# Kernel tuning notes

Hardware: AMD Instinct MI355X
Metric: run time of the kernel (lower is better)

Reference implementation:

```python
import jax, jax.numpy as jnp
import numpy as np

C = 64          # n_channels
NCLS = 10       # output_size
EPS = 1e-5      # GroupNorm eps (torch default)
T0, DT, NSTEPS = 0.0, 0.1, 10  # t0=0, t1=1, dt=0.1 -> 10 fixed RK4 steps


def _gn(x, w, b):
    # GroupNorm(C, C): per-sample, per-channel norm over H,W
    m = x.mean(axis=(2, 3), keepdims=True)
    v = ((x - m) ** 2).mean(axis=(2, 3), keepdims=True)
    return (x - m) * jax.lax.rsqrt(v + EPS) * w[None, :, None, None] + b[None, :, None, None]


def _conv(x, w, b, stride, pad):
    y = jax.lax.conv_general_dilated(x, w, (stride, stride), pad,
                                     dimension_numbers=('NCHW', 'OIHW', 'NCHW'))
    return y + b[None, :, None, None]


def setup_inputs() -> dict:
    key = jax.random.key(0)
    ks = jax.random.split(key, 8)
    rnd = lambda k, shape, s: jax.random.normal(k, shape, jnp.float32) * s
    B = 64
    return dict(
        x=jax.random.normal(ks[0], (B, 1, 130, 130), jnp.float32),
        # downsampler: Conv(1->C,3,1,VALID), GN, ReLU, Conv(C->C,4,2,1), GN, ReLU, Conv(C->C,4,2,1)
        ds_w1=rnd(ks[1], (C, 1, 3, 3), 0.2), ds_b1=jnp.zeros((C,), jnp.float32),
        ds_n1w=jnp.ones((C,), jnp.float32), ds_n1b=jnp.zeros((C,), jnp.float32),
        ds_w2=rnd(ks[2], (C, C, 4, 4), 0.03), ds_b2=jnp.zeros((C,), jnp.float32),
        ds_n2w=jnp.ones((C,), jnp.float32), ds_n2b=jnp.zeros((C,), jnp.float32),
        ds_w3=rnd(ks[3], (C, C, 4, 4), 0.03), ds_b3=jnp.zeros((C,), jnp.float32),
        # ODE RHS: two Conv2d(C+1 -> C, 3, 1, 1) with time channel concat, two GroupNorms
        ode_w1=rnd(ks[4], (C, C + 1, 3, 3), 0.04), ode_b1=jnp.zeros((C,), jnp.float32),
        ode_n1w=jnp.ones((C,), jnp.float32), ode_n1b=jnp.zeros((C,), jnp.float32),
        ode_w2=rnd(ks[5], (C, C + 1, 3, 3), 0.04), ode_b2=jnp.zeros((C,), jnp.float32),
        ode_n2w=jnp.ones((C,), jnp.float32), ode_n2b=jnp.zeros((C,), jnp.float32),
        # classification head: GN, ReLU, GAP, Linear(C -> 10)
        head_nw=jnp.ones((C,), jnp.float32), head_nb=jnp.zeros((C,), jnp.float32),
        head_W=rnd(ks[6], (NCLS, C), 0.1), head_b=jnp.zeros((NCLS,), jnp.float32),
    )


def reference(x, ds_w1, ds_b1, ds_n1w, ds_n1b, ds_w2, ds_b2, ds_n2w, ds_n2b, ds_w3, ds_b3,
              ode_w1, ode_b1, ode_n1w, ode_n1b, ode_w2, ode_b2, ode_n2w, ode_n2b,
              head_nw, head_nb, head_W, head_b):
    P1 = [(1, 1), (1, 1)]
    # ---- downsampler ----
    h = _conv(x, ds_w1, ds_b1, 1, 'VALID')                      # [B,C,128,128]
    h = jax.nn.relu(_gn(h, ds_n1w, ds_n1b))
    h = _conv(h, ds_w2, ds_b2, 2, P1)                           # [B,C,64,64]
    h = jax.nn.relu(_gn(h, ds_n2w, ds_n2b))
    h = _conv(h, ds_w3, ds_b3, 2, P1)                           # [B,C,32,32]

    # ---- ODE layer: fixed-step classic RK4 (tableau_low), 10 steps ----
    def rhs(t, z):
        z = jax.nn.relu(_gn(z, ode_n1w, ode_n1b))
        ts = jnp.full_like(z[:, :1], t)
        z = _conv(jnp.concatenate((ts, z), axis=1), ode_w1, ode_b1, 1, P1)
        z = jax.nn.relu(_gn(z, ode_n2w, ode_n2b))
        ts = jnp.full_like(z[:, :1], t)
        z = _conv(jnp.concatenate((ts, z), axis=1), ode_w2, ode_b2, 1, P1)
        return z

    def step(z, i):
        t = T0 + i * DT
        k1 = rhs(t, z)
        k2 = rhs(t + 0.5 * DT, z + 0.5 * DT * k1)
        k3 = rhs(t + 0.5 * DT, z + 0.5 * DT * k2)
        k4 = rhs(t + DT, z + DT * k3)
        return z + (DT / 6.0) * (k1 + 2.0 * k2 + 2.0 * k3 + k4), None

    h, _ = jax.lax.scan(step, h, jnp.arange(NSTEPS, dtype=jnp.float32))

    # ---- classification head ----
    h = jax.nn.relu(_gn(h, head_nw, head_nb))
    h = h.mean(axis=(2, 3))                                     # AdaptiveAvgPool2d((1,1)) + Flatten
    return h @ head_W.T + head_b                                # [B, 10]
```

## Files before the change

kernel.cpp:

```cpp
#include <hip/hip_runtime.h>

#define BB 64
#define CC 64

typedef __attribute__((ext_vector_type(8))) short short8;
typedef __attribute__((ext_vector_type(4))) short short4v;
typedef __attribute__((ext_vector_type(4))) float f32x4;

__device__ __forceinline__ float bf2f(unsigned short h) {
    unsigned int u = ((unsigned int)h) << 16;
    float f; __builtin_memcpy(&f, &u, 4); return f;
}
__device__ __forceinline__ unsigned short f2bf(float f) {
    unsigned int u; __builtin_memcpy(&u, &f, 4);
    u += 0x7fffu + ((u >> 16) & 1u);
    return (unsigned short)(u >> 16);
}

__global__ __launch_bounds__(256) void conv1stats_kernel(const float* __restrict__ x,
    const float* __restrict__ w1, const float* __restrict__ b1,
    float* __restrict__ ps, float* __restrict__ ps2) {
    __shared__ float sw1[576];
    __shared__ float sb1[64];
    __shared__ float xs[10 * 130];
    int tid = threadIdx.x;
    int qq = blockIdx.x;
    int b = blockIdx.y;
    for (int i = tid; i < 576; i += 256) sw1[i] = w1[i];
    if (tid < 64) sb1[tid] = b1[tid];
    const float* xb = x + (size_t)b * 130 * 130;
    int c = tid >> 2, q = tid & 3;
    float s = 0.f, s2 = 0.f;
    for (int sidx = 0; sidx < 2; sidx++) {
        int row0 = (qq * 2 + sidx) * 8;
        __syncthreads();
        for (int i = tid; i < 1300; i += 256) xs[i] = xb[row0 * 130 + i];
        __syncthreads();
        const float* wc = &sw1[c * 9];
        float bc = sb1[c];
        for (int p = q; p < 1024; p += 4) {
            int y = p >> 7, xx = p & 127;
            float v = bc;
#pragma unroll
            for (int ky = 0; ky < 3; ky++)
#pragma unroll
                for (int kx = 0; kx < 3; kx++)
                    v += xs[(y + ky) * 130 + xx + kx] * wc[ky * 3 + kx];
            s += v; s2 += v * v;
        }
    }
    s  += __shfl_xor(s, 1, 64);  s  += __shfl_xor(s, 2, 64);
    s2 += __shfl_xor(s2, 1, 64); s2 += __shfl_xor(s2, 2, 64);
    if (q == 0) {
        ps [(b * 8 + qq) * 64 + c] = s;
        ps2[(b * 8 + qq) * 64 + c] = s2;
    }
}

__global__ __launch_bounds__(256) void gn1fin_kernel(const float* __restrict__ ps,
    const float* __restrict__ ps2, const float* __restrict__ n1w, const float* __restrict__ n1b,
    float* __restrict__ gn1sc, float* __restrict__ gn1sh) {
    int i = blockIdx.x * 256 + threadIdx.x;
    if (i >= BB * CC) return;
    int c = i & 63, b = i >> 6;
    float s = 0.f, s2 = 0.f;
#pragma unroll
    for (int qq = 0; qq < 8; qq++) {
        s  += ps [(b * 8 + qq) * 64 + c];
        s2 += ps2[(b * 8 + qq) * 64 + c];
    }
    float mean = s / 16384.f;
    float var = s2 / 16384.f - mean * mean;
    float rstd = rsqrtf(var + 1e-5f);
    float sc = rstd * n1w[c];
    gn1sc[i] = sc;
    gn1sh[i] = n1b[c] - mean * sc;
}

__global__ __launch_bounds__(256) void prepack_kernel(const float* __restrict__ w1,
    const float* __restrict__ w2, const float* __restrict__ dw2,
    const float* __restrict__ dw3, unsigned short* __restrict__ Apk,
    float* __restrict__ Stab) {
    int set = blockIdx.y, kc = blockIdx.x, tid = threadIdx.x;
    int nchunk = (set < 2) ? 18 : 32;
    if (kc < nchunk) {
        const float* w = (set == 0) ? w1 : (set == 1) ? w2 : (set == 2) ? dw2 : dw3;
        size_t off = (set == 0) ? 0 : (set == 1) ? 36864 : (set == 2) ? 73728 : 139264;
        for (int e = tid; e < 2048; e += 256) {
            int co = e >> 5, j = e & 31;
            int k = kc * 32 + j;
            int ci = k & 63;
            int tap = k >> 6;
            float val;
            if (set < 2) val = w[(co * 65 + ci + 1) * 9 + tap];
            else         val = w[((co << 6) + ci) * 16 + tap];
            Apk[off + (size_t)kc * 2048 + e] = f2bf(val);
        }
    }
    if (set < 2 && kc == 0) {
        const float* w = set ? w2 : w1;
        for (int t = tid; t < 576; t += 256) {
            int co = t / 9, tap = t % 9;
            Stab[set * 576 + t] = w[(co * 65) * 9 + tap];
        }
    }
}

__global__ __launch_bounds__(256) void ds2mfma_kernel(const float* __restrict__ x,
    const float* __restrict__ w1, const float* __restrict__ b1,
    const float* __restrict__ gn1sc, const float* __restrict__ gn1sh,
    const unsigned short* __restrict__ Apk, const float* __restrict__ bias2,
    unsigned short* __restrict__ h2, float* __restrict__ sums_out) {
    __shared__ unsigned short X[2 * 198 * 64];
    __shared__ float xs[8 * 68];
    __shared__ float sw1[576];
    __shared__ float sb1[64], ssc[64], ssh[64], sb2[64];
    __shared__ float sred[4][64], s2red[4][64];
    int tid = threadIdx.x;
    int b = blockIdx.y;
    int bx = blockIdx.x;
    int xh = bx & 1, sy = bx >> 1;
    int lane = tid & 63, w = tid >> 6;
    int colL = lane & 15, quad = lane >> 4;

    for (int i = tid; i < 576; i += 256) sw1[i] = w1[i];
    if (tid < 64) {
        sb1[tid] = b1[tid];
        ssc[tid] = gn1sc[b * 64 + tid];
        ssh[tid] = gn1sh[b * 64 + tid];
        sb2[tid] = bias2[tid];
    }
    {
        const float* xb = x + (size_t)b * 130 * 130;
        for (int i = tid; i < 544; i += 256) {
            int r = i / 68, cc = i % 68;
            int xr = 4 * sy - 1 + r, xcg = 64 * xh - 1 + cc;
            xs[i] = (xr >= 0 && xr < 130 && xcg >= 0 && xcg < 130) ? xb[xr * 130 + xcg] : 0.f;
        }
    }
    __syncthreads();
    {
        int sub = tid & 7;
        float sbr[8], scr[8], shr[8];
#pragma unroll
        for (int e = 0; e < 8; e++) {
            int c = sub * 8 + e;
            sbr[e] = sb1[c]; scr[e] = ssc[c]; shr[e] = ssh[c];
        }
        for (int i = tid; i < 3168; i += 256) {
            int pidx = i >> 3;
            int ir = pidx / 66, ic = pidx - ir * 66;
            int gy = 4 * sy - 1 + ir, gxg = 64 * xh - 1 + ic;
            short8 o;
            if (gy >= 0 && gy < 128 && gxg >= 0 && gxg < 128) {
#pragma unroll
                for (int e = 0; e < 8; e++) {
                    int c = sub * 8 + e;
                    float v = sbr[e];
#pragma unroll
                    for (int ky = 0; ky < 3; ky++)
#pragma unroll
                        for (int kx = 0; kx < 3; kx++)
                            v += xs[(ir + ky) * 68 + ic + kx] * sw1[c * 9 + ky * 3 + kx];
                    o[e] = (short)f2bf(fmaxf(fmaf(v, scr[e], shr[e]), 0.f));
                }
            } else {
#pragma unroll
                for (int e = 0; e < 8; e++) o[e] = 0;
            }
            int p = ic & 1;
            int psx = ir * 33 + (ic >> 1);
            *(short8*)(X + ((p * 198 + psx) << 6) + ((sub ^ (psx & 7)) << 3)) = o;
        }
    }
    __syncthreads();

    int l = w >> 1, oxb = (w & 1) * 16;
    int oxl = oxb + colL;
    f32x4 acc[4] = {};
    for (int kc = 0; kc < 32; ++kc) {
        int tap = kc >> 1;
        int ky = tap >> 2, kx = tap & 3;
        int chgrp = (kc & 1) * 4 + quad;
        int ir = 2 * l + ky;
        int p = kx & 1;
        int psx = ir * 33 + oxl + (kx >> 1);
        short8 bb = *(const short8*)(X + ((p * 198 + psx) << 6) + ((chgrp ^ (psx & 7)) << 3));
        const unsigned short* ap = Apk + (((kc << 6) + colL) << 5) + (quad << 3);
        short8 a0 = *(const short8*)(ap);
        short8 a1 = *(const short8*)(ap + 512);
        short8 a2 = *(const short8*)(ap + 1024);
        short8 a3 = *(const short8*)(ap + 1536);
        acc[0] = __builtin_amdgcn_mfma_f32_16x16x32_bf16(a0, bb, acc[0], 0, 0, 0);
        acc[1] = __builtin_amdgcn_mfma_f32_16x16x32_bf16(a1, bb, acc[1], 0, 0, 0);
        acc[2] = __builtin_amdgcn_mfma_f32_16x16x32_bf16(a2, bb, acc[2], 0, 0, 0);
        acc[3] = __builtin_amdgcn_mfma_f32_16x16x32_bf16(a3, bb, acc[3], 0, 0, 0);
    }

    float sl[16], s2l[16];
#pragma unroll
    for (int i = 0; i < 16; i++) { sl[i] = 0.f; s2l[i] = 0.f; }
    int oy = 2 * sy + l, oxg = xh * 32 + oxl;
#pragma unroll
    for (int mt = 0; mt < 4; ++mt) {
        int co0 = mt * 16 + quad * 4;
        size_t base = ((size_t)((b * 64 + oy) * 64 + oxg)) * 64 + co0;
        short4v o;
#pragma unroll
        for (int r = 0; r < 4; ++r) {
            unsigned short hh = f2bf(acc[mt][r] + sb2[co0 + r]);
            o[r] = (short)hh;
            float f = bf2f(hh);
            sl[mt * 4 + r] += f; s2l[mt * 4 + r] += f * f;
        }
        *(short4v*)(h2 + base) = o;
    }
#pragma unroll
    for (int idx = 0; idx < 16; ++idx) {
        float s = sl[idx], s2 = s2l[idx];
        s += __shfl_xor(s, 1, 64); s += __shfl_xor(s, 2, 64);
        s += __shfl_xor(s, 4, 64); s += __shfl_xor(s, 8, 64);
        s2 += __shfl_xor(s2, 1, 64); s2 += __shfl_xor(s2, 2, 64);
        s2 += __shfl_xor(s2, 4, 64); s2 += __shfl_xor(s2, 8, 64);
        if (colL == 0) {
            int co = (idx >> 2) * 16 + quad * 4 + (idx & 3);
            sred[w][co] = s; s2red[w][co] = s2;
        }
    }
    __syncthreads();
    if (tid < 64) {
        float s = sred[0][tid] + sred[1][tid] + sred[2][tid] + sred[3][tid];
        float s2 = s2red[0][tid] + s2red[1][tid] + s2red[2][tid] + s2red[3][tid];
        sums_out[(size_t)bx * 8192 + b * 64 + tid] = s;
        sums_out[(size_t)bx * 8192 + 4096 + b * 64 + tid] = s2;
    }
}

__global__ __launch_bounds__(256) void ds3mfma_kernel(const unsigned short* __restrict__ h2,
    const float* __restrict__ sums_in, const float* __restrict__ gw, const float* __restrict__ gb,
    const unsigned short* __restrict__ Apk, const float* __restrict__ bias3,
    float* __restrict__ z, unsigned short* __restrict__ zb, float* __restrict__ sums_out) {
    __shared__ unsigned short X[2 * 198 * 64];
    __shared__ float ssc[64], ssh[64], sb3[64];
    __shared__ float sred[4][64], s2red[4][64];
    int tid = threadIdx.x;
    int b = blockIdx.y, sy = blockIdx.x;
    int lane = tid & 63, w = tid >> 6;
    int colL = lane & 15, quad = lane >> 4;

    if (tid < 64) {
        int c = tid;
        float s = 0.f, s2 = 0.f;
        const float* sp = sums_in + b * 64 + c;
        for (int i = 0; i < 64; i++) { s += sp[(size_t)i * 8192]; s2 += sp[(size_t)i * 8192 + 4096]; }
        float mean = s * (1.f / 4096.f);
        float var = fmaxf(s2 * (1.f / 4096.f) - mean * mean, 0.f);
        float sc = rsqrtf(var + 1e-5f) * gw[c];
        ssc[c] = sc;
        ssh[c] = gb[c] - mean * sc;
        sb3[c] = bias3[c];
    }
    __syncthreads();
    {
        int sub = tid & 7;
        float scr[8], shr[8];
#pragma unroll
        for (int e = 0; e < 8; e++) { scr[e] = ssc[sub * 8 + e]; shr[e] = ssh[sub * 8 + e]; }
        for (int i = tid; i < 3168; i += 256) {
            int pidx = i >> 3;
            int ir = pidx / 66, ic = pidx - ir * 66;
            int gy = 4 * sy - 1 + ir, gx = ic - 1;
            short8 o;
            if (gy >= 0 && gy < 64 && gx >= 0 && gx < 64) {
                short8 d = *(const short8*)(h2 + ((size_t)((b * 64 + gy) * 64 + gx)) * 64 + sub * 8);
#pragma unroll
                for (int e = 0; e < 8; e++) {
                    float f = bf2f((unsigned short)d[e]);
                    o[e] = (short)f2bf(fmaxf(fmaf(f, scr[e], shr[e]), 0.f));
                }
            } else {
#pragma unroll
                for (int e = 0; e < 8; e++) o[e] = 0;
            }
            int p = ic & 1;
            int psx = ir * 33 + (ic >> 1);
            *(short8*)(X + ((p * 198 + psx) << 6) + ((sub ^ (psx & 7)) << 3)) = o;
        }
    }
    __syncthreads();

    int l = w >> 1, oxb = (w & 1) * 16;
    int oxl = oxb + colL;
    f32x4 acc[4] = {};
    for (int kc = 0; kc < 32; ++kc) {
        int tap = kc >> 1;
        int ky = tap >> 2, kx = tap & 3;
        int chgrp = (kc & 1) * 4 + quad;
        int ir = 2 * l + ky;
        int p = kx & 1;
        int psx = ir * 33 + oxl + (kx >> 1);
        short8 bb = *(const short8*)(X + ((p * 198 + psx) << 6) + ((chgrp ^ (psx & 7)) << 3));
        const unsigned short* ap = Apk + (((kc << 6) + colL) << 5) + (quad << 3);
        short8 a0 = *(const short8*)(ap);
        short8 a1 = *(const short8*)(ap + 512);
        short8 a2 = *(const short8*)(ap + 1024);
        short8 a3 = *(const short8*)(ap + 1536);
        acc[0] = __builtin_amdgcn_mfma_f32_16x16x32_bf16(a0, bb, acc[0], 0, 0, 0);
        acc[1] = __builtin_amdgcn_mfma_f32_16x16x32_bf16(a1, bb, acc[1], 0, 0, 0);
        acc[2] = __builtin_amdgcn_mfma_f32_16x16x32_bf16(a2, bb, acc[2], 0, 0, 0);
        acc[3] = __builtin_amdgcn_mfma_f32_16x16x32_bf16(a3, bb, acc[3], 0, 0, 0);
    }

    float sl[16], s2l[16];
#pragma unroll
    for (int i = 0; i < 16; i++) { sl[i] = 0.f; s2l[i] = 0.f; }
    int py = 2 * sy + l;
#pragma unroll
    for (int mt = 0; mt < 4; ++mt) {
        int co0 = mt * 16 + quad * 4;
        size_t base = ((size_t)((b << 10) + py * 32 + oxl)) * 64 + co0;
        f32x4 zv;
        short4v o;
#pragma unroll
        for (int r = 0; r < 4; ++r) {
            float val = acc[mt][r] + sb3[co0 + r];
            zv[r] = val;
            unsigned short hh = f2bf(val);
            o[r] = (short)hh;
            float f = bf2f(hh);
            sl[mt * 4 + r] += f; s2l[mt * 4 + r] += f * f;
        }
        *(f32x4*)(z + base) = zv;
        *(short4v*)(zb + base) = o;
    }
#pragma unroll
    for (int idx = 0; idx < 16; ++idx) {
        float s = sl[idx], s2 = s2l[idx];
        s += __shfl_xor(s, 1, 64); s += __shfl_xor(s, 2, 64);
        s += __shfl_xor(s, 4, 64); s += __shfl_xor(s, 8, 64);
        s2 += __shfl_xor(s2, 1, 64); s2 += __shfl_xor(s2, 2, 64);
        s2 += __shfl_xor(s2, 4, 64); s2 += __shfl_xor(s2, 8, 64);
        if (colL == 0) {
            int co = (idx >> 2) * 16 + quad * 4 + (idx & 3);
            sred[w][co] = s; s2red[w][co] = s2;
        }
    }
    __syncthreads();
    if (tid < 64) {
        float s = sred[0][tid] + sred[1][tid] + sred[2][tid] + sred[3][tid];
        float s2 = s2red[0][tid] + s2red[1][tid] + s2red[2][tid] + s2red[3][tid];
        sums_out[(size_t)sy * 8192 + b * 64 + tid] = s;
        sums_out[(size_t)sy * 8192 + 4096 + b * 64 + tid] = s2;
    }
}

#define CONV_LDS_BYTES 124416
__global__ __launch_bounds__(512, 2) void convmfma_kernel(
    const unsigned short* __restrict__ uin, const float* __restrict__ sums_in, int nsub,
    const float* __restrict__ gw, const float* __restrict__ gb,
    const unsigned short* __restrict__ Apk, const float* __restrict__ stab,
    const float* __restrict__ bias, float t, float aa, int mode,
    float* __restrict__ z, const unsigned short* __restrict__ zbin,
    unsigned short* __restrict__ uout, unsigned short* __restrict__ kacc,
    float* __restrict__ sums_out)
{
    extern __shared__ unsigned short smem[];
    unsigned short* Aw = smem;
    unsigned short* X  = smem + 36864;
    float* fp    = (float*)(smem + 36864 + 21760);
    float* ssc   = fp;        float* ssh   = fp + 64;
    float* tS    = fp + 128;  float* trow0 = fp + 192;  float* trow2 = fp + 256;
    float* tcol0 = fp + 320;  float* tcol2 = fp + 384;
    float* tc00  = fp + 448;  float* tc02  = fp + 512;
    float* tc20  = fp + 576;  float* tc22  = fp + 640;
    float* sred  = fp + 704;
    float* s2red = fp + 1216;

    int tid = threadIdx.x;
    int b = blockIdx.y, strip = blockIdx.x;
    int y0 = strip * 8;
    int lane = tid & 63, w = tid >> 6;
    int colL = lane & 15, quad = lane >> 4;

    {
        f32x4 zz = 0.f;
        for (int i = tid; i < 2720; i += 512) ((f32x4*)X)[i] = zz;
    }
    for (int i = tid; i < 4608; i += 512) ((f32x4*)Aw)[i] = ((const f32x4*)Apk)[i];

    if (tid < 64) {
        int c = tid;
        float s = 0.f, s2 = 0.f;
        const float* sp = sums_in + b * 64 + c;
        for (int i = 0; i < nsub; i++) { s += sp[(size_t)i * 8192]; s2 += sp[(size_t)i * 8192 + 4096]; }
        float mean = s * (1.f / 1024.f);
        float var = fmaxf(s2 * (1.f / 1024.f) - mean * mean, 0.f);
        float sc = rsqrtf(var + 1e-5f) * gw[c];
        ssc[c] = sc;
        ssh[c] = gb[c] - mean * sc;
    } else if (tid < 128) {
        int co = tid - 64;
        float w0[9];
#pragma unroll
        for (int k = 0; k < 9; k++) w0[k] = stab[co * 9 + k] * t;
        tS[co] = bias[co] + w0[0]+w0[1]+w0[2]+w0[3]+w0[4]+w0[5]+w0[6]+w0[7]+w0[8];
        trow0[co] = w0[0] + w0[1] + w0[2];
        trow2[co] = w0[6] + w0[7] + w0[8];
        tcol0[co] = w0[0] + w0[3] + w0[6];
        tcol2[co] = w0[2] + w0[5] + w0[8];
        tc00[co] = w0[0]; tc02[co] = w0[2]; tc20[co] = w0[6]; tc22[co] = w0[8];
    }
    __syncthreads();

    {
        int sub = tid & 7;
        float scr[8], shr[8];
#pragma unroll
        for (int e = 0; e < 8; e++) { scr[e] = ssc[sub * 8 + e]; shr[e] = ssh[sub * 8 + e]; }
#pragma unroll
        for (int it = 0; it < 5; ++it) {
            int pidx = (tid >> 3) + it * 64;
            int r = pidx >> 5, xc = pidx & 31;
            int gy = y0 - 1 + r;
            if (gy < 0 || gy > 31) continue;
            int gp = (b << 10) + gy * 32 + xc;
            short8 d = *(const short8*)(uin + (size_t)gp * 64 + sub * 8);
            short8 o;
#pragma unroll
            for (int e = 0; e < 8; e++) {
                float f = bf2f((unsigned short)d[e]);
                o[e] = (short)f2bf(fmaxf(fmaf(f, scr[e], shr[e]), 0.f));
            }
            int psx = r * 34 + xc + 1;
            *(short8*)(X + (psx << 6) + ((sub ^ (psx & 7)) << 3)) = o;
        }
    }
    __syncthreads();

    f32x4 acc[4][2] = {};
    for (int kc = 0; kc < 18; ++kc) {
        int tap = kc >> 1;
        int dy = tap / 3, dx = tap % 3;
        int chgrp = (kc & 1) * 4 + quad;
        int ps0 = (w + dy) * 34 + colL + dx;
        int ps1 = ps0 + 16;
        short8 bb0 = *(const short8*)(X + (ps0 << 6) + ((chgrp ^ (ps0 & 7)) << 3));
        short8 bb1 = *(const short8*)(X + (ps1 << 6) + ((chgrp ^ (ps1 & 7)) << 3));
        const unsigned short* ap = Aw + (((kc << 6) + colL) << 5) + (quad << 3);
        short8 a0 = *(const short8*)(ap);
        short8 a1 = *(const short8*)(ap + 512);
        short8 a2 = *(const short8*)(ap + 1024);
        short8 a3 = *(const short8*)(ap + 1536);
        acc[0][0] = __builtin_amdgcn_mfma_f32_16x16x32_bf16(a0, bb0, acc[0][0], 0, 0, 0);
        acc[0][1] = __builtin_amdgcn_mfma_f32_16x16x32_bf16(a0, bb1, acc[0][1], 0, 0, 0);
        acc[1][0] = __builtin_amdgcn_mfma_f32_16x16x32_bf16(a1, bb0, acc[1][0], 0, 0, 0);
        acc[1][1] = __builtin_amdgcn_mfma_f32_16x16x32_bf16(a1, bb1, acc[1][1], 0, 0, 0);
        acc[2][0] = __builtin_amdgcn_mfma_f32_16x16x32_bf16(a2, bb0, acc[2][0], 0, 0, 0);
        acc[2][1] = __builtin_amdgcn_mfma_f32_16x16x32_bf16(a2, bb1, acc[2][1], 0, 0, 0);
        acc[3][0] = __builtin_amdgcn_mfma_f32_16x16x32_bf16(a3, bb0, acc[3][0], 0, 0, 0);
        acc[3][1] = __builtin_amdgcn_mfma_f32_16x16x32_bf16(a3, bb1, acc[3][1], 0, 0, 0);
    }

    float sl[16], s2l[16];
#pragma unroll
    for (int i = 0; i < 16; i++) { sl[i] = 0.f; s2l[i] = 0.f; }
    int py = y0 + w;
    bool by0 = (py == 0), by1 = (py == 31);
#pragma unroll
    for (int nt = 0; nt < 2; ++nt) {
        int px = nt * 16 + colL;
        bool bx0 = (px == 0), bx1 = (px == 31);
#pragma unroll
        for (int mt = 0; mt < 4; ++mt) {
            int co0 = mt * 16 + quad * 4;
            float vout[4];
#pragma unroll
            for (int r = 0; r < 4; ++r) {
                int co = co0 + r;
                float val = acc[mt][nt][r] + tS[co];
                if (by0) { val -= trow0[co]; if (bx0) val += tc00[co]; if (bx1) val += tc02[co]; }
                if (by1) { val -= trow2[co]; if (bx0) val += tc20[co]; if (bx1) val += tc22[co]; }
                if (bx0) val -= tcol0[co];
                if (bx1) val -= tcol2[co];
                vout[r] = val;
            }
            size_t base = ((size_t)((b << 10) + py * 32 + px)) * 64 + co0;
            if (mode == 3) {
                short4v o;
#pragma unroll
                for (int r = 0; r < 4; ++r) {
                    unsigned short hh = f2bf(vout[r]);
                    o[r] = (short)hh;
                    float f = bf2f(hh);
                    sl[mt * 4 + r] += f; s2l[mt * 4 + r] += f * f;
                }
                *(short4v*)(uout + base) = o;
            } else if (mode == 2) {
                short4v kv = *(const short4v*)(kacc + base);
                f32x4 zv = *(const f32x4*)(z + base);
                short4v o;
#pragma unroll
                for (int r = 0; r < 4; ++r) {
                    float zn = zv[r] + aa * (bf2f((unsigned short)kv[r]) + vout[r]);
                    zv[r] = zn;
                    unsigned short hh = f2bf(zn);
                    o[r] = (short)hh;
                    float f = bf2f(hh);
                    sl[mt * 4 + r] += f; s2l[mt * 4 + r] += f * f;
                }
                *(f32x4*)(z + base) = zv;
                *(short4v*)(uout + base) = o;
            } else {
                short4v zs = *(const short4v*)(zbin + base);
                short4v ko, o;
                if (mode == 1) {
                    short4v kv = *(const short4v*)(kacc + base);
#pragma unroll
                    for (int r = 0; r < 4; ++r)
                        ko[r] = (short)f2bf(bf2f((unsigned short)kv[r]) + 2.f * vout[r]);
                } else {
#pragma unroll
                    for (int r = 0; r < 4; ++r) ko[r] = (short)f2bf(vout[r]);
                }
                *(short4v*)(kacc + base) = ko;
#pragma unroll
                for (int r = 0; r < 4; ++r) {
                    float zf = bf2f((unsigned short)zs[r]);
                    unsigned short hh = f2bf(zf + aa * vout[r]);
                    o[r] = (short)hh;
                    float f = bf2f(hh);
                    sl[mt * 4 + r] += f; s2l[mt * 4 + r] += f * f;
                }
                *(short4v*)(uout + base) = o;
            }
        }
    }
#pragma unroll
    for (int idx = 0; idx < 16; ++idx) {
        float s = sl[idx], s2 = s2l[idx];
        s += __shfl_xor(s, 1, 64); s += __shfl_xor(s, 2, 64);
        s += __shfl_xor(s, 4, 64); s += __shfl_xor(s, 8, 64);
        s2 += __shfl_xor(s2, 1, 64); s2 += __shfl_xor(s2, 2, 64);
        s2 += __shfl_xor(s2, 4, 64); s2 += __shfl_xor(s2, 8, 64);
        if (colL == 0) {
            int co = (idx >> 2) * 16 + quad * 4 + (idx & 3);
            sred[w * 64 + co] = s; s2red[w * 64 + co] = s2;
        }
    }
    __syncthreads();
    if (tid < 64) {
        float s = 0.f, s2 = 0.f;
#pragma unroll
        for (int i = 0; i < 8; i++) { s += sred[i * 64 + tid]; s2 += s2red[i * 64 + tid]; }
        sums_out[(size_t)strip * 8192 + b * 64 + tid] = s;
        sums_out[(size_t)strip * 8192 + 4096 + b * 64 + tid] = s2;
    }
}

__global__ __launch_bounds__(256) void headgap_kernel(const float* __restrict__ z,
    const float* __restrict__ w, const float* __restrict__ b, float* __restrict__ pooled) {
    __shared__ float r1[4][64], r2[4][64];
    __shared__ float scs[64], shs[64];
    int bq = blockIdx.x, tid = threadIdx.x;
    int c = tid & 63, g = tid >> 6;
    float s = 0.f, s2 = 0.f;
    for (int p = g; p < 1024; p += 4) {
        float v = z[((size_t)((bq << 10) + p)) * 64 + c];
        s += v; s2 += v * v;
    }
    r1[g][c] = s; r2[g][c] = s2;
    __syncthreads();
    if (tid < 64) {
        float ts = r1[0][tid] + r1[1][tid] + r1[2][tid] + r1[3][tid];
        float ts2 = r2[0][tid] + r2[1][tid] + r2[2][tid] + r2[3][tid];
        float mean = ts / 1024.f;
        float var = fmaxf(ts2 / 1024.f - mean * mean, 0.f);
        float sc = rsqrtf(var + 1e-5f) * w[tid];
        scs[tid] = sc;
        shs[tid] = b[tid] - mean * sc;
    }
    __syncthreads();
    float sc = scs[c], sh = shs[c];
    float r = 0.f;
    for (int p = g; p < 1024; p += 4)
        r += fmaxf(fmaf(z[((size_t)((bq << 10) + p)) * 64 + c], sc, sh), 0.f);
    r1[g][c] = r;
    __syncthreads();
    if (tid < 64)
        pooled[bq * 64 + tid] = (r1[0][tid] + r1[1][tid] + r1[2][tid] + r1[3][tid]) / 1024.f;
}

__global__ __launch_bounds__(256) void headfc_kernel(const float* __restrict__ pooled,
    const float* __restrict__ W, const float* __restrict__ bias, float* __restrict__ out) {
    int i = blockIdx.x * 256 + threadIdx.x;
    if (i < 640) {
        int b = i / 10, j = i % 10;
        float a = bias[j];
        const float* p = pooled + b * 64;
        const float* wj = W + j * 64;
#pragma unroll 8
        for (int c = 0; c < 64; c++) a += p[c] * wj[c];
        out[i] = a;
    }
}

extern "C" void kernel_launch(void* const* d_in, const int* in_sizes, int n_in,
                              void* d_out, int out_size, void* d_ws, size_t ws_size,
                              hipStream_t stream) {
    const float* x      = (const float*)d_in[0];
    const float* ds_w1  = (const float*)d_in[1];
    const float* ds_b1  = (const float*)d_in[2];
    const float* ds_n1w = (const float*)d_in[3];
    const float* ds_n1b = (const float*)d_in[4];
    const float* ds_w2  = (const float*)d_in[5];
    const float* ds_b2  = (const float*)d_in[6];
    const float* ds_n2w = (const float*)d_in[7];
    const float* ds_n2b = (const float*)d_in[8];
    const float* ds_w3  = (const float*)d_in[9];
    const float* ds_b3  = (const float*)d_in[10];
    const float* ode_w1 = (const float*)d_in[11];
    const float* ode_b1 = (const float*)d_in[12];
    const float* ode_n1w= (const float*)d_in[13];
    const float* ode_n1b= (const float*)d_in[14];
    const float* ode_w2 = (const float*)d_in[15];
    const float* ode_b2 = (const float*)d_in[16];
    const float* ode_n2w= (const float*)d_in[17];
    const float* ode_n2b= (const float*)d_in[18];
    const float* head_nw= (const float*)d_in[19];
    const float* head_nb= (const float*)d_in[20];
    const float* head_W = (const float*)d_in[21];
    const float* head_b = (const float*)d_in[22];

    const size_t NZ = (size_t)BB * CC * 32 * 32;
    float* ws = (float*)d_ws;
    float*          z     = ws;
    unsigned short* zb    = (unsigned short*)(ws + NZ);
    unsigned short* u     = (unsigned short*)(ws + 3 * NZ / 2);
    unsigned short* v     = (unsigned short*)(ws + 2 * NZ);
    unsigned short* kacc  = (unsigned short*)(ws + 5 * NZ / 2);
    unsigned short* h2    = u;
    float*          apf   = ws + 7 * NZ / 2;
    unsigned short* Apk   = (unsigned short*)apf;
    float*          Stab  = apf + 102400;
    float*          ds2s  = Stab + 1152;
    float*          zsum  = ds2s + (size_t)64 * 8192;
    float*          osl   = zsum + (size_t)16 * 8192;
    float*          ps    = osl + (size_t)80 * 32768;
    float*          ps2   = ps + 32768;
    float*          gn1sc = ps2 + 32768;
    float*          gn1sh = gn1sc + 4096;
    float*          pooled= gn1sh + 4096;

    auto OSL = [&](int j) { return osl + (size_t)j * 32768; };

    hipFuncSetAttribute(reinterpret_cast<const void*>(convmfma_kernel),
                        hipFuncAttributeMaxDynamicSharedMemorySize, CONV_LDS_BYTES);

    prepack_kernel<<<dim3(32, 4), 256, 0, stream>>>(ode_w1, ode_w2, ds_w2, ds_w3, Apk, Stab);

    conv1stats_kernel<<<dim3(8, BB), 256, 0, stream>>>(x, ds_w1, ds_b1, ps, ps2);
    gn1fin_kernel<<<16, 256, 0, stream>>>(ps, ps2, ds_n1w, ds_n1b, gn1sc, gn1sh);
    ds2mfma_kernel<<<dim3(64, BB), 256, 0, stream>>>(x, ds_w1, ds_b1, gn1sc, gn1sh,
        Apk + 73728, ds_b2, h2, ds2s);
    ds3mfma_kernel<<<dim3(16, BB), 256, 0, stream>>>(h2, ds2s, ds_n2w, ds_n2b,
        Apk + 139264, ds_b3, z, zb, zsum);

    const unsigned short* AP1 = Apk;
    const unsigned short* AP2 = Apk + 36864;
    const float* ST1 = Stab;
    const float* ST2 = Stab + 576;
    const float c6 = 0.1f / 6.0f;
    dim3 cgrid(4, BB);
    for (int i = 0; i < 10; i++) {
        float t0 = 0.1f * (float)i;
        int j = 8 * i;
        const float* s0 = (i == 0) ? zsum : OSL(j - 1);
        int n0 = (i == 0) ? 16 : 4;
        convmfma_kernel<<<cgrid, 512, CONV_LDS_BYTES, stream>>>(zb, s0, n0, ode_n1w, ode_n1b,
            AP1, ST1, ode_b1, t0, 0.f, 3, z, zb, v, kacc, OSL(j));
        convmfma_kernel<<<cgrid, 512, CONV_LDS_BYTES, stream>>>(v, OSL(j), 4, ode_n2w, ode_n2b,
            AP2, ST2, ode_b2, t0, 0.05f, 0, z, zb, u, kacc, OSL(j + 1));
        convmfma_kernel<<<cgrid, 512, CONV_LDS_BYTES, stream>>>(u, OSL(j + 1), 4, ode_n1w, ode_n1b,
            AP1, ST1, ode_b1, t0 + 0.05f, 0.f, 3, z, zb, v, kacc, OSL(j + 2));
        convmfma_kernel<<<cgrid, 512, CONV_LDS_BYTES, stream>>>(v, OSL(j + 2), 4, ode_n2w, ode_n2b,
            AP2, ST2, ode_b2, t0 + 0.05f, 0.05f, 1, z, zb, u, kacc, OSL(j + 3));
        convmfma_kernel<<<cgrid, 512, CONV_LDS_BYTES, stream>>>(u, OSL(j + 3), 4, ode_n1w, ode_n1b,
            AP1, ST1, ode_b1, t0 + 0.05f, 0.f, 3, z, zb, v, kacc, OSL(j + 4));
        convmfma_kernel<<<cgrid, 512, CONV_LDS_BYTES, stream>>>(v, OSL(j + 4), 4, ode_n2w, ode_n2b,
            AP2, ST2, ode_b2, t0 + 0.05f, 0.1f, 1, z, zb, u, kacc, OSL(j + 5));
        convmfma_kernel<<<cgrid, 512, CONV_LDS_BYTES, stream>>>(u, OSL(j + 5), 4, ode_n1w, ode_n1b,
            AP1, ST1, ode_b1, t0 + 0.1f, 0.f, 3, z, zb, v, kacc, OSL(j + 6));
        convmfma_kernel<<<cgrid, 512, CONV_LDS_BYTES, stream>>>(v, OSL(j + 6), 4, ode_n2w, ode_n2b,
            AP2, ST2, ode_b2, t0 + 0.1f, c6, 2, z, zb, zb, kacc, OSL(j + 7));
    }

    headgap_kernel<<<BB, 256, 0, stream>>>(z, head_nw, head_nb, pooled);
    headfc_kernel<<<3, 256, 0, stream>>>(pooled, head_W, head_b, (float*)d_out);
}
```

Measured before the change: 2.242 ms.

## Pad LDS weight rows and prefetch conv inputs and epilogue operands early

Weight rows in LDS are padded to a 40-element stride to cut bank conflicts on the A-fragment reads in the MFMA loop. The per-block input activations are loaded into registers before the weight copy and zero-fill, so the global latency overlaps that setup. The epilogue operands (z, kacc, zbin) are also loaded before the MFMA loop so their latency hides behind the compute. The cost is more LDS per block and many more live registers across the main loop, which risks spills under the 512-thread, 2-block launch bound.

Result: faster. 2.195 ms (-2.1%).

```diff
diff --git a/kernel.cpp b/kernel.cpp
--- a/kernel.cpp
+++ b/kernel.cpp
@@ -354,7 +354,8 @@
     }
 }
 
-#define CONV_LDS_BYTES 124416
+#define APAD 40
+#define CONV_LDS_BYTES 142592
 __global__ __launch_bounds__(512, 2) void convmfma_kernel(
     const unsigned short* __restrict__ uin, const float* __restrict__ sums_in, int nsub,
     const float* __restrict__ gw, const float* __restrict__ gb,
@@ -366,8 +367,8 @@
 {
     extern __shared__ unsigned short smem[];
     unsigned short* Aw = smem;
-    unsigned short* X  = smem + 36864;
-    float* fp    = (float*)(smem + 36864 + 21760);
+    unsigned short* X  = smem + 46080;
+    float* fp    = (float*)(smem + 67840);
     float* ssc   = fp;        float* ssh   = fp + 64;
     float* tS    = fp + 128;  float* trow0 = fp + 192;  float* trow2 = fp + 256;
     float* tcol0 = fp + 320;  float* tcol2 = fp + 384;
@@ -381,12 +382,30 @@
     int y0 = strip * 8;
     int lane = tid & 63, w = tid >> 6;
     int colL = lane & 15, quad = lane >> 4;
+    int sub = tid & 7;
+
+    short8 dpre[5];
+    int pr[5], pxc[5];
+    bool pok[5];
+#pragma unroll
+    for (int it = 0; it < 5; ++it) {
+        int pidx = (tid >> 3) + it * 64;
+        int r = pidx >> 5, xc = pidx & 31;
+        int gy = y0 - 1 + r;
+        pr[it] = r; pxc[it] = xc;
+        pok[it] = (gy >= 0 && gy <= 31);
+        if (pok[it])
+            dpre[it] = *(const short8*)(uin + ((size_t)((b << 10) + gy * 32 + xc)) * 64 + sub * 8);
+    }
 
     {
         f32x4 zz = 0.f;
         for (int i = tid; i < 2720; i += 512) ((f32x4*)X)[i] = zz;
     }
-    for (int i = tid; i < 4608; i += 512) ((f32x4*)Aw)[i] = ((const f32x4*)Apk)[i];
+    for (int i = tid; i < 4608; i += 512) {
+        int row = i >> 2, part = i & 3;
+        *(f32x4*)(Aw + row * APAD + part * 8) = ((const f32x4*)Apk)[i];
+    }
 
     if (tid < 64) {
         int c = tid;
@@ -413,27 +432,45 @@
     __syncthreads();
 
     {
-        int sub = tid & 7;
         float scr[8], shr[8];
 #pragma unroll
         for (int e = 0; e < 8; e++) { scr[e] = ssc[sub * 8 + e]; shr[e] = ssh[sub * 8 + e]; }
 #pragma unroll
         for (int it = 0; it < 5; ++it) {
-            int pidx = (tid >> 3) + it * 64;
-            int r = pidx >> 5, xc = pidx & 31;
-            int gy = y0 - 1 + r;
-            if (gy < 0 || gy > 31) continue;
-            int gp = (b << 10) + gy * 32 + xc;
-            short8 d = *(const short8*)(uin + (size_t)gp * 64 + sub * 8);
+            if (!pok[it]) continue;
+            short8 d = dpre[it];
             short8 o;
 #pragma unroll
             for (int e = 0; e < 8; e++) {
                 float f = bf2f((unsigned short)d[e]);
                 o[e] = (short)f2bf(fmaxf(fmaf(f, scr[e], shr[e]), 0.f));
             }
-            int psx = r * 34 + xc + 1;
+            int psx = pr[it] * 34 + pxc[it] + 1;
             *(short8*)(X + (psx << 6) + ((sub ^ (psx & 7)) << 3)) = o;
         }
+    }
+
+    int py = y0 + w;
+    short4v preZb[8], preK[8];
+    f32x4 preZ[8];
+    if (mode == 2) {
+#pragma unroll
+        for (int nt = 0; nt < 2; ++nt)
+#pragma unroll
+            for (int mt = 0; mt < 4; ++mt) {
+                size_t base = ((size_t)((b << 10) + py * 32 + nt * 16 + colL)) * 64 + mt * 16 + quad * 4;
+                preK[nt * 4 + mt] = *(const short4v*)(kacc + base);
+                preZ[nt * 4 + mt] = *(const f32x4*)(z + base);
+            }
+    } else if (mode != 3) {
+#pragma unroll
+        for (int nt = 0; nt < 2; ++nt)
+#pragma unroll
+            for (int mt = 0; mt < 4; ++mt) {
+                size_t base = ((size_t)((b << 10) + py * 32 + nt * 16 + colL)) * 64 + mt * 16 + quad * 4;
+                preZb[nt * 4 + mt] = *(const short4v*)(zbin + base);
+                if (mode == 1) preK[nt * 4 + mt] = *(const short4v*)(kacc + base);
+            }
     }
     __syncthreads();
 
@@ -446,11 +483,11 @@
         int ps1 = ps0 + 16;
         short8 bb0 = *(const short8*)(X + (ps0 << 6) + ((chgrp ^ (ps0 & 7)) << 3));
         short8 bb1 = *(const short8*)(X + (ps1 << 6) + ((chgrp ^ (ps1 & 7)) << 3));
-        const unsigned short* ap = Aw + (((kc << 6) + colL) << 5) + (quad << 3);
+        const unsigned short* ap = Aw + ((kc << 6) + colL) * APAD + (quad << 3);
         short8 a0 = *(const short8*)(ap);
-        short8 a1 = *(const short8*)(ap + 512);
-        short8 a2 = *(const short8*)(ap + 1024);
-        short8 a3 = *(const short8*)(ap + 1536);
+        short8 a1 = *(const short8*)(ap + 16 * APAD);
+        short8 a2 = *(const short8*)(ap + 32 * APAD);
+        short8 a3 = *(const short8*)(ap + 48 * APAD);
         acc[0][0] = __builtin_amdgcn_mfma_f32_16x16x32_bf16(a0, bb0, acc[0][0], 0, 0, 0);
         acc[0][1] = __builtin_amdgcn_mfma_f32_16x16x32_bf16(a0, bb1, acc[0][1], 0, 0, 0);
         acc[1][0] = __builtin_amdgcn_mfma_f32_16x16x32_bf16(a1, bb0, acc[1][0], 0, 0, 0);
@@ -464,7 +501,6 @@
     float sl[16], s2l[16];
 #pragma unroll
     for (int i = 0; i < 16; i++) { sl[i] = 0.f; s2l[i] = 0.f; }
-    int py = y0 + w;
     bool by0 = (py == 0), by1 = (py == 31);
 #pragma unroll
     for (int nt = 0; nt < 2; ++nt) {
@@ -473,6 +509,7 @@
 #pragma unroll
         for (int mt = 0; mt < 4; ++mt) {
             int co0 = mt * 16 + quad * 4;
+            int pi = nt * 4 + mt;
             float vout[4];
 #pragma unroll
             for (int r = 0; r < 4; ++r) {
@@ -496,8 +533,8 @@
                 }
                 *(short4v*)(uout + base) = o;
             } else if (mode == 2) {
-                short4v kv = *(const short4v*)(kacc + base);
-                f32x4 zv = *(const f32x4*)(z + base);
+                f32x4 zv = preZ[pi];
+                short4v kv = preK[pi];
                 short4v o;
 #pragma unroll
                 for (int r = 0; r < 4; ++r) {
@@ -511,10 +548,10 @@
                 *(f32x4*)(z + base) = zv;
                 *(short4v*)(uout + base) = o;
             } else {
-                short4v zs = *(const short4v*)(zbin + base);
+                short4v zs = preZb[pi];
                 short4v ko, o;
                 if (mode == 1) {
-                    short4v kv = *(const short4v*)(kacc + base);
+                    short4v kv = preK[pi];
 #pragma unroll
                     for (int r = 0; r < 4; ++r)
                         ko[r] = (short)f2bf(bf2f((unsigned short)kv[r]) + 2.f * vout[r]);
```
